# Performance work log

Measured on AMD Instinct MI355X. Metric: run time of the kernel, lower is better.

## Reference

```python
import jax, jax.numpy as jnp
import numpy as np

B, T, D = 64, 1024, 512      # batch, listener time, 2*listener_hidden
H = 512                      # speller_hidden_dim
M = 256                      # mlp_dim_in_attention
C = 63                       # output_class_dim
S = 64                       # max_label_len (decode steps)
INV_SQRT_2PI = 0.3989422804014327


def setup_inputs() -> dict:
    key = jax.random.key(0)
    ks = jax.random.split(key, 16)
    def lin(k, out_d, in_d, scale=1.0):
        return jax.random.normal(k, (out_d, in_d), jnp.float32) * (scale / np.sqrt(in_d))
    listener_feature = jax.random.normal(ks[0], (B, T, D), jnp.float32)
    labels = jax.random.randint(ks[1], (B, S), 0, C)
    ground_truth = jax.nn.one_hot(labels, C, dtype=jnp.float32)
    return {
        'listener_feature': listener_feature,
        'ground_truth': ground_truth,
        'phi_w': lin(ks[2], M, D, 0.5), 'phi_b': jnp.zeros((M,), jnp.float32),
        'psi_w': lin(ks[3], M, D, 0.5), 'psi_b': jnp.zeros((M,), jnp.float32),
        'w_ih0': lin(ks[4], 4 * H, C + H), 'w_hh0': lin(ks[5], 4 * H, H),
        'b_ih0': jnp.zeros((4 * H,), jnp.float32), 'b_hh0': jnp.zeros((4 * H,), jnp.float32),
        'w_ih1': lin(ks[6], 4 * H, H), 'w_hh1': lin(ks[7], 4 * H, H),
        'b_ih1': jnp.zeros((4 * H,), jnp.float32), 'b_hh1': jnp.zeros((4 * H,), jnp.float32),
        'char_w': lin(ks[8], C, 2 * H), 'char_b': jnp.zeros((C,), jnp.float32),
    }


def _lstm_cell(x, h, c, w_ih, w_hh, b_ih, b_hh):
    g = x @ w_ih.T + b_ih + h @ w_hh.T + b_hh
    i, f, gg, o = jnp.split(g, 4, axis=-1)  # torch gate order i,f,g,o
    c_new = jax.nn.sigmoid(f) * c + jax.nn.sigmoid(i) * jnp.tanh(gg)
    h_new = jax.nn.sigmoid(o) * jnp.tanh(c_new)
    return h_new, c_new


def _copula_score(energy):
    # energy: [B, T]. Gaussian marginal pdf * bivariate Gaussian copula density of
    # adjacent columns (columns 0 and T-1 keep copula factor 1, as in source loop).
    pdf = jnp.exp(-0.5 * energy * energy) * INV_SQRT_2PI
    a = energy[:, :-2]   # column i-1 for i in 1..T-2
    b = energy[:, 1:-1]  # column i
    am = a - a.mean(axis=0)
    bm = b - b.mean(axis=0)
    r = (am * bm).sum(axis=0) / jnp.sqrt((am * am).sum(axis=0) * (bm * bm).sum(axis=0) + 1e-12)
    det = 1.0 - r * r  # det of 2x2 correlation matrix
    det_s = jnp.maximum(det, 1e-6)
    quad = r * r * (a * a + b * b) - 2.0 * r * a * b
    cop = jnp.exp(-0.5 * quad / det_s) / jnp.sqrt(det_s)
    bad = (det < 0.01) | jnp.all(a == b, axis=0)
    cop = jnp.where(bad, 10.0, cop)
    coppdf = jnp.ones_like(energy).at[:, 1:-1].set(cop)
    ef1 = pdf * coppdf
    # source falls back to softmax(energy) if any column is all-zero (batch>3 here);
    # copula path goes through numpy in torch, i.e. it is detached from autograd.
    any_zero_col = jnp.any(jnp.all(energy == 0.0, axis=0))
    return jnp.where(any_zero_col,
                     jax.nn.softmax(energy, axis=-1),
                     jax.nn.softmax(jax.lax.stop_gradient(ef1), axis=-1))


def _speller(listener_feature, ground_truth, phi_w, phi_b, psi_w, psi_b,
             w_ih0, w_hh0, b_ih0, b_hh0, w_ih1, w_hh1, b_ih1, b_hh1,
             char_w, char_b):
    comp_listener = jax.nn.relu(jnp.einsum('btd,md->btm', listener_feature, psi_w) + psi_b)

    def step(carry, gt_t):
        h0, c0, h1, c1, rnn_in = carry
        h0, c0 = _lstm_cell(rnn_in, h0, c0, w_ih0, w_hh0, b_ih0, b_hh0)
        h1, c1 = _lstm_cell(h0, h1, c1, w_ih1, w_hh1, b_ih1, b_hh1)
        dec = h1  # [B, H] top-layer rnn_output
        comp_dec = jax.nn.relu(dec @ phi_w.T + phi_b)            # [B, M]
        energy = jnp.einsum('bm,btm->bt', comp_dec, comp_listener)
        att = _copula_score(energy)                              # [B, T]
        context = jnp.einsum('bt,btd->bd', att, listener_feature)
        concat = jnp.concatenate([dec, context], axis=-1)        # [B, 2H]
        raw_pred = jax.nn.log_softmax(concat @ char_w.T + char_b, axis=-1)
        new_in = jnp.concatenate([gt_t, context], axis=-1)       # teacher forcing
        return (h0, c0, h1, c1, new_in), (raw_pred, att)

    z = jnp.zeros((B, H), listener_feature.dtype)
    onehot0 = jnp.zeros((B, C), listener_feature.dtype).at[:, 0].set(1.0)
    init_in = jnp.concatenate([onehot0, listener_feature[:, 0, :]], axis=-1)
    gt_seq = jnp.transpose(ground_truth, (1, 0, 2))  # [S, B, C]
    _, (preds, atts) = jax.lax.scan(step, (z, z, z, z, init_in), gt_seq)
    return preds, atts  # [S,B,C] log-probs, [S,B,T] attention scores


def reference(listener_feature, ground_truth, phi_w, phi_b, psi_w, psi_b,
              w_ih0, w_hh0, b_ih0, b_hh0, w_ih1, w_hh1, b_ih1, b_hh1,
              char_w, char_b):
    return _speller(listener_feature, ground_truth, phi_w, phi_b, psi_w, psi_b,
                    w_ih0, w_hh0, b_ih0, b_hh0, w_ih1, w_hh1, b_ih1, b_hh1,
                    char_w, char_b)
```

## Files before the change

### kernel.cpp

```cpp
#include <hip/hip_runtime.h>
#include <hip/hip_bf16.h>
#include <math.h>

#define B_ 64
#define T_ 1024
#define D_ 512
#define H_ 512
#define M_ 256
#define CC 63
#define SS 64
#define INV_SQRT_2PI 0.3989422804014327f

typedef __attribute__((ext_vector_type(8))) short short8v;
typedef __attribute__((ext_vector_type(4))) float f32x4;

static __device__ __forceinline__ float bf2f(unsigned short u) {
    unsigned int x = ((unsigned int)u) << 16;
    return __uint_as_float(x);
}
static __device__ __forceinline__ unsigned short f2bf(float f) {
    unsigned int x = __float_as_uint(f);
    unsigned int r = (x + 0x7fff + ((x >> 16) & 1)) >> 16;
    return (unsigned short)r;
}
static __device__ __forceinline__ float sigm(float x) {
    return 1.f / (1.f + __expf(-x));
}
static __device__ __forceinline__ float wsum64(float v) {
    for (int o = 32; o > 0; o >>= 1) v += __shfl_xor(v, o, 64);
    return v;
}


__global__ __launch_bounds__(256) void k_conv(const float* __restrict__ src,
        unsigned short* __restrict__ dst, int n4) {
    int stride = gridDim.x * 256;
    for (int i = blockIdx.x * 256 + threadIdx.x; i < n4; i += stride) {
        float4 v = ((const float4*)src)[i];
        ushort4 o;
        o.x = f2bf(v.x); o.y = f2bf(v.y); o.z = f2bf(v.z); o.w = f2bf(v.w);
        ((ushort4*)dst)[i] = o;
    }
}

__global__ __launch_bounds__(256) void k_gemm_mfma(
        const unsigned short* __restrict__ Abf,
        const unsigned short* __restrict__ Bbf,
        const float* __restrict__ psib,
        unsigned short* __restrict__ clT) {
    __shared__ unsigned short As[64 * 40];
    __shared__ unsigned short Bs[64 * 40];
    __shared__ unsigned short Os[64 * 72];
    int tid = threadIdx.x;
    int p0 = (blockIdx.x >> 2) * 64;
    int m0 = (blockIdx.x & 3) * 64;
    int w = tid >> 6, l = tid & 63;
    int wp = (w & 1) * 32, wm = (w >> 1) * 32;
    f32x4 acc[2][2] = {};
    int srow = tid >> 2, sc = (tid & 3) * 8;
    for (int k0 = 0; k0 < 512; k0 += 32) {
        __syncthreads();
        *(short8v*)&As[srow * 40 + sc] = *(const short8v*)&Abf[(size_t)(p0 + srow) * 512 + k0 + sc];
        *(short8v*)&Bs[srow * 40 + sc] = *(const short8v*)&Bbf[(size_t)(m0 + srow) * 512 + k0 + sc];
        __syncthreads();
        int koff = (l >> 4) * 8;
        int rlo = l & 15;
        short8v a0 = *(short8v*)&As[(wp + rlo) * 40 + koff];
        short8v a1 = *(short8v*)&As[(wp + 16 + rlo) * 40 + koff];
        short8v b0 = *(short8v*)&Bs[(wm + rlo) * 40 + koff];
        short8v b1 = *(short8v*)&Bs[(wm + 16 + rlo) * 40 + koff];
        acc[0][0] = __builtin_amdgcn_mfma_f32_16x16x32_bf16(a0, b0, acc[0][0], 0, 0, 0);
        acc[0][1] = __builtin_amdgcn_mfma_f32_16x16x32_bf16(a0, b1, acc[0][1], 0, 0, 0);
        acc[1][0] = __builtin_amdgcn_mfma_f32_16x16x32_bf16(a1, b0, acc[1][0], 0, 0, 0);
        acc[1][1] = __builtin_amdgcn_mfma_f32_16x16x32_bf16(a1, b1, acc[1][1], 0, 0, 0);
    }
    __syncthreads();
#pragma unroll
    for (int pi = 0; pi < 2; ++pi)
#pragma unroll
        for (int mi = 0; mi < 2; ++mi)
#pragma unroll
            for (int r = 0; r < 4; ++r) {
                int tl = wp + pi * 16 + (l >> 4) * 4 + r;
                int ml = wm + mi * 16 + (l & 15);
                float v = fmaxf(acc[pi][mi][r] + psib[m0 + ml], 0.f);
                Os[ml * 72 + tl] = f2bf(v);
            }
    __syncthreads();
    int b = p0 >> 10, t0 = p0 & 1023;
    int mm = tid >> 2, c16 = (tid & 3) * 16;
    short8v v0 = *(short8v*)&Os[mm * 72 + c16];
    short8v v1 = *(short8v*)&Os[mm * 72 + c16 + 8];
    size_t base = ((size_t)(b * 256 + m0 + mm)) * 1024 + t0 + c16;
    *(short8v*)&clT[base] = v0;
    *(short8v*)&clT[base + 8] = v1;
}

__global__ __launch_bounds__(256) void k_init(const float* __restrict__ Lf,
        const float* __restrict__ gt,
        float* gtT, float* h0a, float* h1a, float* c0, float* c1,
        float* ctxT, float* ctxb) {
    int tid = threadIdx.x, blk = blockIdx.x;
    if (blk < 64) {
        for (int r = tid; r < CC * 64; r += 256) {
            int k = r >> 6, b = r & 63;
            gtT[blk * (CC * 64) + r] = gt[(b * SS + blk) * CC + k];
        }
    } else {
        int idx = (blk - 64) * 256 + tid;
        h0a[idx] = 0.f; h1a[idx] = 0.f; c0[idx] = 0.f; c1[idx] = 0.f;
        int d = idx >> 6, b = idx & 63;
        float v = Lf[(size_t)b * (T_ * D_) + d];
        ctxT[idx] = v;
        ctxb[b * 512 + d] = v;
    }
}


__global__ __launch_bounds__(256) void k_lstm0(
        int s, const float* __restrict__ gtT, const float* __restrict__ ctxT,
        const float* __restrict__ h0in, float* __restrict__ h0out,
        float* __restrict__ c0,
        const float* __restrict__ wih0, const float* __restrict__ whh0,
        const float* __restrict__ bih0, const float* __restrict__ bhh0,
        int* __restrict__ colZero) {
    __shared__ float xs[4096];
    __shared__ float wsm[16 * 68];
    __shared__ float ex[16 * 64];
    int tid = threadIdx.x, uid = blockIdx.x;
    int r = tid >> 4, tb = tid & 15;
    float a0 = 0.f, a1 = 0.f, a2 = 0.f, a3 = 0.f;
    for (int kc = 0; kc < 17; ++kc) {
        int k0 = kc * 64;
        __syncthreads();
#pragma unroll
        for (int i = 0; i < 4; ++i) {
            int e4 = i * 256 + tid;
            int kk = e4 >> 4, b4 = (e4 & 15) * 4;
            int k = k0 + kk;
            float4 v;
            if (k < 63) {
                if (s > 0) v = *(const float4*)&gtT[(s - 1) * 4032 + k * 64 + b4];
                else { float o1 = (k == 0) ? 1.f : 0.f; v = make_float4(o1, o1, o1, o1); }
            } else if (k < 575)  v = *(const float4*)&ctxT[(k - 63) * 64 + b4];
            else if (k < 1087)   v = *(const float4*)&h0in[(k - 575) * 64 + b4];
            else                 v = make_float4(0.f, 0.f, 0.f, 0.f);
            *(float4*)&xs[kk * 64 + b4] = v;
        }
#pragma unroll
        for (int i = 0; i < 4; ++i) {
            int lidx = i * 256 + tid;
            int rr = lidx >> 6, kk = lidx & 63;
            int k = k0 + kk;
            int g2 = rr >> 2, uu = rr & 3;
            int jj = g2 * 512 + uid * 4 + uu;
            float wv;
            if (k < 575)       wv = wih0[(size_t)jj * 575 + k];
            else if (k < 1087) wv = whh0[(size_t)jj * 512 + (k - 575)];
            else               wv = 0.f;
            wsm[rr * 68 + kk] = wv;
        }
        __syncthreads();
        const float* wsr = &wsm[r * 68];
        const float* xsr = &xs[tb * 4];
#pragma unroll
        for (int kk = 0; kk < 64; ++kk) {
            float wv = wsr[kk];
            float4 x4 = *(const float4*)&xsr[kk * 64];
            a0 = fmaf(wv, x4.x, a0);
            a1 = fmaf(wv, x4.y, a1);
            a2 = fmaf(wv, x4.z, a2);
            a3 = fmaf(wv, x4.w, a3);
        }
    }
    {
        int g2 = r >> 2, uu = r & 3;
        int j = g2 * 512 + uid * 4 + uu;
        float bias = bih0[j] + bhh0[j];
        __syncthreads();
        *(float4*)&ex[r * 64 + tb * 4] =
            make_float4(a0 + bias, a1 + bias, a2 + bias, a3 + bias);
    }
    __syncthreads();
    {
        int ui = tid >> 6, b = tid & 63;
        float gi = ex[(0 * 4 + ui) * 64 + b];
        float gf = ex[(1 * 4 + ui) * 64 + b];
        float gg = ex[(2 * 4 + ui) * 64 + b];
        float go = ex[(3 * 4 + ui) * 64 + b];
        int u = uid * 4 + ui;
        float cv = c0[u * 64 + b];
        float cn = sigm(gf) * cv + sigm(gi) * tanhf(gg);
        float hn = sigm(go) * tanhf(cn);
        c0[u * 64 + b] = cn;
        h0out[u * 64 + b] = hn;
    }
    if (uid == 0) {
        for (int i = tid; i < 1024; i += 256) colZero[i] = 1;
    }
}

__global__ __launch_bounds__(256) void k_lstm1(
        const float* __restrict__ h0cur, const float* __restrict__ h1in,
        float* __restrict__ h1out, float* __restrict__ c1,
        float* __restrict__ h1bout,
        const float* __restrict__ wih1, const float* __restrict__ whh1,
        const float* __restrict__ bih1, const float* __restrict__ bhh1) {
    __shared__ float xs[4096];
    __shared__ float wsm[16 * 68];
    __shared__ float ex[16 * 64];
    int tid = threadIdx.x, uid = blockIdx.x;
    int r = tid >> 4, tb = tid & 15;
    float a0 = 0.f, a1 = 0.f, a2 = 0.f, a3 = 0.f;
    for (int kc = 0; kc < 16; ++kc) {
        int k0 = kc * 64;
        __syncthreads();
#pragma unroll
        for (int i = 0; i < 4; ++i) {
            int e4 = i * 256 + tid;
            int kk = e4 >> 4, b4 = (e4 & 15) * 4;
            int k = k0 + kk;
            float4 v = (k < 512) ? *(const float4*)&h0cur[k * 64 + b4]
                                 : *(const float4*)&h1in[(k - 512) * 64 + b4];
            *(float4*)&xs[kk * 64 + b4] = v;
        }
#pragma unroll
        for (int i = 0; i < 4; ++i) {
            int lidx = i * 256 + tid;
            int rr = lidx >> 6, kk = lidx & 63;
            int k = k0 + kk;
            int g2 = rr >> 2, uu = rr & 3;
            int jj = g2 * 512 + uid * 4 + uu;
            float wv = (k < 512) ? wih1[(size_t)jj * 512 + k]
                                 : whh1[(size_t)jj * 512 + (k - 512)];
            wsm[rr * 68 + kk] = wv;
        }
        __syncthreads();
        const float* wsr = &wsm[r * 68];
        const float* xsr = &xs[tb * 4];
#pragma unroll
        for (int kk = 0; kk < 64; ++kk) {
            float wv = wsr[kk];
            float4 x4 = *(const float4*)&xsr[kk * 64];
            a0 = fmaf(wv, x4.x, a0);
            a1 = fmaf(wv, x4.y, a1);
            a2 = fmaf(wv, x4.z, a2);
            a3 = fmaf(wv, x4.w, a3);
        }
    }
    {
        int g2 = r >> 2, uu = r & 3;
        int j = g2 * 512 + uid * 4 + uu;
        float bias = bih1[j] + bhh1[j];
        __syncthreads();
        *(float4*)&ex[r * 64 + tb * 4] =
            make_float4(a0 + bias, a1 + bias, a2 + bias, a3 + bias);
    }
    __syncthreads();
    {
        int ui = tid >> 6, b = tid & 63;
        float gi = ex[(0 * 4 + ui) * 64 + b];
        float gf = ex[(1 * 4 + ui) * 64 + b];
        float gg = ex[(2 * 4 + ui) * 64 + b];
        float go = ex[(3 * 4 + ui) * 64 + b];
        int u = uid * 4 + ui;
        float cv = c1[u * 64 + b];
        float cn = sigm(gf) * cv + sigm(gi) * tanhf(gg);
        float hn = sigm(go) * tanhf(cn);
        c1[u * 64 + b] = cn;
        h1out[u * 64 + b] = hn;
        h1bout[b * 512 + u] = hn;
    }
}

__global__ __launch_bounds__(256) void k_phi(
        const float* __restrict__ h1u,
        const float* __restrict__ phiw, const float* __restrict__ phib,
        float* __restrict__ cdb) {
    __shared__ float xs[4096];
    __shared__ float wsm[32 * 68];
    int tid = threadIdx.x;
    int m0 = blockIdx.x * 32;
    int mr = tid >> 3, bq = tid & 7;
    float bias = phib[m0 + mr];
    float acc[8] = {bias, bias, bias, bias, bias, bias, bias, bias};
    for (int kc = 0; kc < 8; ++kc) {
        int k0 = kc * 64;
        __syncthreads();
#pragma unroll
        for (int i = 0; i < 4; ++i) {
            int idx4 = i * 256 + tid;
            int kk = idx4 >> 4, b4 = (idx4 & 15) * 4;
            *(float4*)&xs[kk * 64 + b4] = *(const float4*)&h1u[(k0 + kk) * 64 + b4];
        }
#pragma unroll
        for (int i = 0; i < 2; ++i) {
            int idx4 = i * 256 + tid;
            int mm = idx4 >> 4, kk4 = (idx4 & 15) * 4;
            *(float4*)&wsm[mm * 68 + kk4] = *(const float4*)&phiw[(size_t)(m0 + mm) * 512 + k0 + kk4];
        }
        __syncthreads();
        const float* wr = &wsm[mr * 68];
#pragma unroll
        for (int kk = 0; kk < 64; ++kk) {
            float wv = wr[kk];
            const float* xp = &xs[kk * 64 + bq * 8];
#pragma unroll
            for (int j = 0; j < 8; ++j)
                acc[j] = fmaf(xp[j], wv, acc[j]);
        }
    }
#pragma unroll
    for (int j = 0; j < 8; ++j)
        cdb[(bq * 8 + j) * 256 + m0 + mr] = fmaxf(acc[j], 0.f);
}

__global__ __launch_bounds__(128) void k_energy(
        const float* __restrict__ cdb,
        const unsigned short* __restrict__ clT,
        float* __restrict__ energy_bt, float* __restrict__ energyT,
        int* __restrict__ colZero) {
    __shared__ float cdl[256];
    int tid = threadIdx.x;
    int b = blockIdx.x >> 3, tc = blockIdx.x & 7;
    cdl[tid] = cdb[b * 256 + tid];
    cdl[128 + tid] = cdb[b * 256 + 128 + tid];
    __syncthreads();
    int t = tc * 128 + tid;
    float e = 0.f;
    const unsigned short* base = clT + ((size_t)(b * 256)) * 1024 + t;
#pragma unroll 16
    for (int m = 0; m < 256; ++m)
        e = fmaf(cdl[m], bf2f(base[(size_t)m * 1024]), e);
    energyT[t * 64 + b] = e;
    energy_bt[b * 1024 + t] = e;
    if (e != 0.f) colZero[t] = 0;
}

__global__ __launch_bounds__(256) void k_cop(
        const float* __restrict__ energyT,
        float* __restrict__ rS, float* __restrict__ dsS, int* __restrict__ badS) {
    int tid = threadIdx.x;
    int wv = tid >> 6, b = tid & 63;
    int t = blockIdx.x * 4 + wv;
    if (t >= 1 && t < 1023) {
        float e = energyT[t * 64 + b];
        float a = energyT[(t - 1) * 64 + b];
        float ma = wsum64(a) * (1.f / 64.f);
        float mb = wsum64(e) * (1.f / 64.f);
        float am = a - ma, bm = e - mb;
        float sab = wsum64(am * bm);
        float saa = wsum64(am * am);
        float sbb = wsum64(bm * bm);
        int aeq = __all(a == e);
        float r = sab / sqrtf(saa * sbb + 1e-12f);
        float det = 1.f - r * r;
        int bad = (det < 0.01f || aeq) ? 1 : 0;
        float ds = fmaxf(det, 1e-6f);
        if (b == 0) { rS[t] = r; dsS[t] = ds; badS[t] = bad; }
    }
}

__global__ __launch_bounds__(256) void k_soft(
        int doSM, int s, int prow,
        const float* __restrict__ energy_bt, const int* __restrict__ colZero,
        const float* __restrict__ rS, const float* __restrict__ dsS,
        const int* __restrict__ badS,
        const float* __restrict__ h1bp, const float* __restrict__ ctxb,
        const float* __restrict__ charw, const float* __restrict__ charb,
        float* __restrict__ preds, float* __restrict__ atts,
        float* __restrict__ attbuf) {
    __shared__ float e_l[1024];
    __shared__ float red[256];
    __shared__ int zred[256];
    __shared__ float cpx[1024];
    __shared__ float lgs[64];
    int tid = threadIdx.x, b = blockIdx.x;
    if (doSM) {
        *(float4*)&e_l[tid * 4] = *(const float4*)&energy_bt[b * 1024 + tid * 4];
        int z = colZero[tid] | colZero[256 + tid] | colZero[512 + tid] | colZero[768 + tid];
        zred[tid] = z;
        __syncthreads();
        for (int o = 128; o > 0; o >>= 1) {
            if (tid < o) zred[tid] |= zred[tid + o];
            __syncthreads();
        }
        int zf = zred[0];
        float4 rv = *(const float4*)&rS[tid * 4];
        float4 dv = *(const float4*)&dsS[tid * 4];
        int4 bv = *(const int4*)&badS[tid * 4];
        float rvv[4] = {rv.x, rv.y, rv.z, rv.w};
        float dvv[4] = {dv.x, dv.y, dv.z, dv.w};
        int bvv[4] = {bv.x, bv.y, bv.z, bv.w};
        float vals[4];
#pragma unroll
        for (int i = 0; i < 4; ++i) {
            int t = tid * 4 + i;
            float e = e_l[t];
            if (zf) {
                vals[i] = e;
            } else {
                float cp;
                if (t == 0 || t == 1023) cp = 1.f;
                else if (bvv[i]) cp = 10.f;
                else {
                    float a = e_l[t - 1];
                    float r = rvv[i], ds = dvv[i];
                    float quad = r * r * (a * a + e * e) - 2.f * r * a * e;
                    cp = __expf(-0.5f * quad / ds) / sqrtf(ds);
                }
                vals[i] = __expf(-0.5f * e * e) * INV_SQRT_2PI * cp;
            }
        }
        float lm = fmaxf(fmaxf(vals[0], vals[1]), fmaxf(vals[2], vals[3]));
        red[tid] = lm;
        __syncthreads();
        for (int o = 128; o > 0; o >>= 1) {
            if (tid < o) red[tid] = fmaxf(red[tid], red[tid + o]);
            __syncthreads();
        }
        float M = red[0];
        __syncthreads();
        float e0 = __expf(vals[0] - M), e1 = __expf(vals[1] - M);
        float e2 = __expf(vals[2] - M), e3 = __expf(vals[3] - M);
        red[tid] = e0 + e1 + e2 + e3;
        __syncthreads();
        for (int o = 128; o > 0; o >>= 1) {
            if (tid < o) red[tid] += red[tid + o];
            __syncthreads();
        }
        float inv = 1.f / red[0];
        float4 a4 = make_float4(e0 * inv, e1 * inv, e2 * inv, e3 * inv);
        *(float4*)&attbuf[b * 1024 + tid * 4] = a4;
        *(float4*)&atts[((size_t)s * B_ + b) * 1024 + tid * 4] = a4;
    }
    if (prow >= 0) {
        __syncthreads();
        for (int i = tid; i < 1024; i += 256)
            cpx[i] = (i < 512) ? h1bp[b * 512 + i] : ctxb[b * 512 + (i - 512)];
        __syncthreads();
        int c = tid >> 2, kl = tid & 3;
        float p = 0.f;
        if (c < 63) {
            const float4* cw = (const float4*)&charw[(size_t)c * 1024 + kl * 256];
            const float4* cx = (const float4*)&cpx[kl * 256];
#pragma unroll
            for (int q = 0; q < 64; ++q) {
                float4 w4 = cw[q], x4 = cx[q];
                p = fmaf(x4.x, w4.x, p); p = fmaf(x4.y, w4.y, p);
                p = fmaf(x4.z, w4.z, p); p = fmaf(x4.w, w4.w, p);
            }
        }
        p += __shfl_xor(p, 1, 64); p += __shfl_xor(p, 2, 64);
        if (kl == 0 && c < 63) lgs[c] = p + charb[c];
        if (tid == 0) lgs[63] = -1e30f;
        __syncthreads();
        if (tid < 64) {
            float lg = (tid < 63) ? lgs[tid] : -1e30f;
            float mx = lg;
            for (int o = 32; o > 0; o >>= 1) mx = fmaxf(mx, __shfl_xor(mx, o, 64));
            float ex2 = (tid < 63) ? __expf(lg - mx) : 0.f;
            float sume = wsum64(ex2);
            if (tid < 63)
                preds[((size_t)prow * B_ + b) * CC + tid] = lg - mx - __logf(sume);
        }
    }
}

__global__ __launch_bounds__(256) void k_ctx(
        const float* __restrict__ attbuf, const unsigned short* __restrict__ Lbf,
        float* __restrict__ ctxT, float* __restrict__ ctxb) {
    __shared__ float att[1056];
    __shared__ float red2[256];
    int tid = threadIdx.x;
    int b = blockIdx.x >> 3, dq = blockIdx.x & 7, d0 = dq * 64;
    {
        float4 a4 = *(const float4*)&attbuf[b * 1024 + tid * 4];
        int t = tid * 4;
        int pk = t + (t >> 5);
        att[pk] = a4.x; att[pk + 1] = a4.y; att[pk + 2] = a4.z; att[pk + 3] = a4.w;
    }
    __syncthreads();
    int tc = tid >> 3, dg = tid & 7;
    const unsigned short* Lb = Lbf + (size_t)b * 524288 + (size_t)tc * 32 * 512 + d0 + dg * 8;
    float acc[8] = {0.f, 0.f, 0.f, 0.f, 0.f, 0.f, 0.f, 0.f};
#pragma unroll
    for (int i = 0; i < 32; ++i) {
        float wv = att[tc * 33 + i];
        short8v v = *(const short8v*)(Lb + (size_t)i * 512);
        acc[0] = fmaf(wv, bf2f((unsigned short)v[0]), acc[0]);
        acc[1] = fmaf(wv, bf2f((unsigned short)v[1]), acc[1]);
        acc[2] = fmaf(wv, bf2f((unsigned short)v[2]), acc[2]);
        acc[3] = fmaf(wv, bf2f((unsigned short)v[3]), acc[3]);
        acc[4] = fmaf(wv, bf2f((unsigned short)v[4]), acc[4]);
        acc[5] = fmaf(wv, bf2f((unsigned short)v[5]), acc[5]);
        acc[6] = fmaf(wv, bf2f((unsigned short)v[6]), acc[6]);
        acc[7] = fmaf(wv, bf2f((unsigned short)v[7]), acc[7]);
    }
#pragma unroll
    for (int j = 0; j < 8; ++j) {
        acc[j] += __shfl_xor(acc[j], 8, 64);
        acc[j] += __shfl_xor(acc[j], 16, 64);
        acc[j] += __shfl_xor(acc[j], 32, 64);
    }
    int w = tid >> 6;
    if ((tid & 56) == 0) {
#pragma unroll
        for (int j = 0; j < 8; ++j) red2[w * 64 + dg * 8 + j] = acc[j];
    }
    __syncthreads();
    if (tid < 64) {
        float cv = red2[tid] + red2[64 + tid] + red2[128 + tid] + red2[192 + tid];
        ctxT[(d0 + tid) * 64 + b] = cv;
        ctxb[b * 512 + d0 + tid] = cv;
    }
}

extern "C" void kernel_launch(void* const* d_in, const int* in_sizes, int n_in,
                              void* d_out, int out_size, void* d_ws, size_t ws_size,
                              hipStream_t stream) {
    const float* Lf   = (const float*)d_in[0];
    const float* gt   = (const float*)d_in[1];
    const float* phiw = (const float*)d_in[2];
    const float* phib = (const float*)d_in[3];
    const float* psiw = (const float*)d_in[4];
    const float* psib = (const float*)d_in[5];
    const float* wih0 = (const float*)d_in[6];
    const float* whh0 = (const float*)d_in[7];
    const float* bih0 = (const float*)d_in[8];
    const float* bhh0 = (const float*)d_in[9];
    const float* wih1 = (const float*)d_in[10];
    const float* whh1 = (const float*)d_in[11];
    const float* bih1 = (const float*)d_in[12];
    const float* bhh1 = (const float*)d_in[13];
    const float* charw = (const float*)d_in[14];
    const float* charb = (const float*)d_in[15];

    float* preds = (float*)d_out;
    float* atts  = (float*)d_out + (size_t)SS * B_ * CC;

    char* ws = (char*)d_ws;
    size_t off = 0;
    auto alloc = [&](size_t bytes) { size_t o = off; off = (off + bytes + 255) & ~(size_t)255; return o; };
    unsigned short* clT = (unsigned short*)(ws + alloc((size_t)B_ * M_ * T_ * 2));
    unsigned short* Lbf = (unsigned short*)(ws + alloc((size_t)B_ * T_ * D_ * 2));
    unsigned short* psibf = (unsigned short*)(ws + alloc((size_t)M_ * D_ * 2));
    float* gtT      = (float*)(ws + alloc((size_t)SS * CC * 64 * 4));
    float* h0p0     = (float*)(ws + alloc(H_ * B_ * 4));
    float* h0p1     = (float*)(ws + alloc(H_ * B_ * 4));
    float* h1p0     = (float*)(ws + alloc(H_ * B_ * 4));
    float* h1p1     = (float*)(ws + alloc(H_ * B_ * 4));
    float* hb0      = (float*)(ws + alloc(H_ * B_ * 4));
    float* hb1      = (float*)(ws + alloc(H_ * B_ * 4));
    float* c0       = (float*)(ws + alloc(H_ * B_ * 4));
    float* c1       = (float*)(ws + alloc(H_ * B_ * 4));
    float* ctxT     = (float*)(ws + alloc(H_ * B_ * 4));
    float* ctxb     = (float*)(ws + alloc(H_ * B_ * 4));
    float* cdb      = (float*)(ws + alloc(B_ * M_ * 4));
    float* energy_bt = (float*)(ws + alloc(B_ * T_ * 4));
    float* energyT   = (float*)(ws + alloc(B_ * T_ * 4));
    float* rS       = (float*)(ws + alloc(T_ * 4));
    float* dsS      = (float*)(ws + alloc(T_ * 4));
    int* badS       = (int*)(ws + alloc(T_ * 4));
    int* colZero    = (int*)(ws + alloc(T_ * 4));
    float* attbuf   = (float*)(ws + alloc(B_ * T_ * 4));

    k_conv<<<2048, 256, 0, stream>>>(Lf, Lbf, (B_ * T_ * D_) / 4);
    k_conv<<<128, 256, 0, stream>>>(psiw, psibf, (M_ * D_) / 4);
    k_gemm_mfma<<<4096, 256, 0, stream>>>(Lbf, psibf, psib, clT);
    k_init<<<192, 256, 0, stream>>>(Lf, gt, gtT, h0p0, h1p0, c0, c1, ctxT, ctxb);

    float* h0p[2] = {h0p0, h0p1};
    float* h1p[2] = {h1p0, h1p1};
    float* hb[2]  = {hb0, hb1};
    for (int s = 0; s < SS; ++s) {
        int pi = s & 1, po = pi ^ 1;
        k_lstm0<<<128, 256, 0, stream>>>(s, gtT, ctxT, h0p[pi], h0p[po], c0,
                                         wih0, whh0, bih0, bhh0, colZero);
        k_lstm1<<<128, 256, 0, stream>>>(h0p[po], h1p[pi], h1p[po], c1, hb[pi],
                                         wih1, whh1, bih1, bhh1);
        k_phi<<<8, 256, 0, stream>>>(h1p[po], phiw, phib, cdb);
        k_energy<<<512, 128, 0, stream>>>(cdb, clT, energy_bt, energyT, colZero);
        k_cop<<<256, 256, 0, stream>>>(energyT, rS, dsS, badS);
        k_soft<<<64, 256, 0, stream>>>(1, s, s - 1, energy_bt, colZero, rS, dsS, badS,
                                       hb[pi ^ 1], ctxb, charw, charb,
                                       preds, atts, attbuf);
        k_ctx<<<512, 256, 0, stream>>>(attbuf, Lbf, ctxT, ctxb);
    }
    k_soft<<<64, 256, 0, stream>>>(0, SS - 1, SS - 1, energy_bt, colZero, rS, dsS, badS,
                                   hb[1], ctxb, charw, charb, preds, atts, attbuf);
}
```

Measured before the change: 8.794 ms.

## Move char prediction into extra lstm0 blocks and vectorize energy loads

```diff
diff --git a/kernel.cpp b/kernel.cpp
--- a/kernel.cpp
+++ b/kernel.cpp
@@ -123,11 +123,50 @@
         float* __restrict__ c0,
         const float* __restrict__ wih0, const float* __restrict__ whh0,
         const float* __restrict__ bih0, const float* __restrict__ bhh0,
-        int* __restrict__ colZero) {
+        int* __restrict__ colZero,
+        const float* __restrict__ h1bp, const float* __restrict__ ctxb,
+        const float* __restrict__ charw, const float* __restrict__ charb,
+        float* __restrict__ preds) {
     __shared__ float xs[4096];
     __shared__ float wsm[16 * 68];
     __shared__ float ex[16 * 64];
+    __shared__ float lgs[64];
     int tid = threadIdx.x, uid = blockIdx.x;
+    if (uid >= 128) {
+        if (s > 0) {
+            int b = uid - 128;
+            float* cpx = xs;
+            for (int i = tid; i < 1024; i += 256)
+                cpx[i] = (i < 512) ? h1bp[b * 512 + i] : ctxb[b * 512 + (i - 512)];
+            __syncthreads();
+            int c = tid >> 2, kl = tid & 3;
+            float p = 0.f;
+            if (c < 63) {
+                const float4* cw = (const float4*)&charw[(size_t)c * 1024 + kl * 256];
+                const float4* cx = (const float4*)&cpx[kl * 256];
+#pragma unroll
+                for (int q = 0; q < 64; ++q) {
+                    float4 w4 = cw[q], x4 = cx[q];
+                    p = fmaf(x4.x, w4.x, p); p = fmaf(x4.y, w4.y, p);
+                    p = fmaf(x4.z, w4.z, p); p = fmaf(x4.w, w4.w, p);
+                }
+            }
+            p += __shfl_xor(p, 1, 64); p += __shfl_xor(p, 2, 64);
+            if (kl == 0 && c < 63) lgs[c] = p + charb[c];
+            if (tid == 0) lgs[63] = -1e30f;
+            __syncthreads();
+            if (tid < 64) {
+                float lg = (tid < 63) ? lgs[tid] : -1e30f;
+                float mx = lg;
+                for (int o = 32; o > 0; o >>= 1) mx = fmaxf(mx, __shfl_xor(mx, o, 64));
+                float ex2 = (tid < 63) ? __expf(lg - mx) : 0.f;
+                float sume = wsum64(ex2);
+                if (tid < 63)
+                    preds[((size_t)(s - 1) * B_ + b) * CC + tid] = lg - mx - __logf(sume);
+            }
+        }
+        return;
+    }
     int r = tid >> 4, tb = tid & 15;
     float a0 = 0.f, a1 = 0.f, a2 = 0.f, a3 = 0.f;
     for (int kc = 0; kc < 17; ++kc) {
@@ -315,26 +354,42 @@
         cdb[(bq * 8 + j) * 256 + m0 + mr] = fmaxf(acc[j], 0.f);
 }
 
-__global__ __launch_bounds__(128) void k_energy(
+__global__ __launch_bounds__(64) void k_energy(
         const float* __restrict__ cdb,
         const unsigned short* __restrict__ clT,
         float* __restrict__ energy_bt, float* __restrict__ energyT,
         int* __restrict__ colZero) {
     __shared__ float cdl[256];
     int tid = threadIdx.x;
-    int b = blockIdx.x >> 3, tc = blockIdx.x & 7;
-    cdl[tid] = cdb[b * 256 + tid];
-    cdl[128 + tid] = cdb[b * 256 + 128 + tid];
+    int b = blockIdx.x >> 1, half = blockIdx.x & 1;
+#pragma unroll
+    for (int j = 0; j < 4; ++j)
+        cdl[j * 64 + tid] = cdb[b * 256 + j * 64 + tid];
     __syncthreads();
-    int t = tc * 128 + tid;
-    float e = 0.f;
-    const unsigned short* base = clT + ((size_t)(b * 256)) * 1024 + t;
-#pragma unroll 16
-    for (int m = 0; m < 256; ++m)
-        e = fmaf(cdl[m], bf2f(base[(size_t)m * 1024]), e);
-    energyT[t * 64 + b] = e;
-    energy_bt[b * 1024 + t] = e;
-    if (e != 0.f) colZero[t] = 0;
+    int t8 = half * 512 + tid * 8;
+    float e[8] = {0.f, 0.f, 0.f, 0.f, 0.f, 0.f, 0.f, 0.f};
+    const unsigned short* base = clT + ((size_t)(b * 256)) * 1024 + t8;
+#pragma unroll 8
+    for (int m = 0; m < 256; ++m) {
+        short8v v = *(const short8v*)(base + (size_t)m * 1024);
+        float c = cdl[m];
+        e[0] = fmaf(c, bf2f((unsigned short)v[0]), e[0]);
+        e[1] = fmaf(c, bf2f((unsigned short)v[1]), e[1]);
+        e[2] = fmaf(c, bf2f((unsigned short)v[2]), e[2]);
+        e[3] = fmaf(c, bf2f((unsigned short)v[3]), e[3]);
+        e[4] = fmaf(c, bf2f((unsigned short)v[4]), e[4]);
+        e[5] = fmaf(c, bf2f((unsigned short)v[5]), e[5]);
+        e[6] = fmaf(c, bf2f((unsigned short)v[6]), e[6]);
+        e[7] = fmaf(c, bf2f((unsigned short)v[7]), e[7]);
+    }
+#pragma unroll
+    for (int j = 0; j < 8; ++j) {
+        int t = t8 + j;
+        energyT[t * 64 + b] = e[j];
+        if (e[j] != 0.f) colZero[t] = 0;
+    }
+    *(float4*)&energy_bt[b * 1024 + t8] = make_float4(e[0], e[1], e[2], e[3]);
+    *(float4*)&energy_bt[b * 1024 + t8 + 4] = make_float4(e[4], e[5], e[6], e[7]);
 }
 
 __global__ __launch_bounds__(256) void k_cop(
@@ -575,15 +630,16 @@
     float* hb[2]  = {hb0, hb1};
     for (int s = 0; s < SS; ++s) {
         int pi = s & 1, po = pi ^ 1;
-        k_lstm0<<<128, 256, 0, stream>>>(s, gtT, ctxT, h0p[pi], h0p[po], c0,
-                                         wih0, whh0, bih0, bhh0, colZero);
+        k_lstm0<<<192, 256, 0, stream>>>(s, gtT, ctxT, h0p[pi], h0p[po], c0,
+                                         wih0, whh0, bih0, bhh0, colZero,
+                                         hb[po], ctxb, charw, charb, preds);
         k_lstm1<<<128, 256, 0, stream>>>(h0p[po], h1p[pi], h1p[po], c1, hb[pi],
                                          wih1, whh1, bih1, bhh1);
         k_phi<<<8, 256, 0, stream>>>(h1p[po], phiw, phib, cdb);
-        k_energy<<<512, 128, 0, stream>>>(cdb, clT, energy_bt, energyT, colZero);
+        k_energy<<<128, 64, 0, stream>>>(cdb, clT, energy_bt, energyT, colZero);
         k_cop<<<256, 256, 0, stream>>>(energyT, rS, dsS, badS);
-        k_soft<<<64, 256, 0, stream>>>(1, s, s - 1, energy_bt, colZero, rS, dsS, badS,
-                                       hb[pi ^ 1], ctxb, charw, charb,
+        k_soft<<<64, 256, 0, stream>>>(1, s, -1, energy_bt, colZero, rS, dsS, badS,
+                                       hb[po], ctxb, charw, charb,
                                        preds, atts, attbuf);
         k_ctx<<<512, 256, 0, stream>>>(attbuf, Lbf, ctxT, ctxb);
     }
```

After: 8.803 ms, median of 2. About the same (+0.1%).
